# Optimization experiments

Hardware: AMD Instinct MI355X
Metric: run time of the kernel (lower is better)

The kernel has to match this reference:

```python
import jax, jax.numpy as jnp
import numpy as np

B, N, A = 8, 16384, 7
NUM_GROUP = 1024   # npoint / G
GROUP_SIZE = 32    # knn k / M


def setup_inputs() -> dict:
    key = jax.random.key(0)
    xyz = jax.random.uniform(key, (B, N, A), dtype=jnp.float32)
    return {"xyz": xyz}


def _farthest_point_sample(xyz, npoint):
    # xyz: [B, N, A]; distances computed on first 3 dims only.
    b, n, a = xyz.shape
    coords = xyz[:, :, :3]
    batch = jnp.arange(b)
    # Deterministic start index (original uses randint; any start is a valid FPS seed).
    init = (jnp.full((b, n), 1e10, dtype=xyz.dtype), jnp.zeros((b,), dtype=jnp.int32))

    def step(carry, _):
        distance, farthest = carry
        centroid = xyz[batch, farthest]                      # [B, A]
        d = jnp.sum((coords - centroid[:, None, :3]) ** 2, -1)  # [B, N]
        distance = jnp.minimum(distance, d)                  # masked update == min
        new_farthest = jnp.argmax(distance, axis=-1).astype(jnp.int32)
        return (distance, new_farthest), (farthest, centroid)

    _, (idxs, cents) = jax.lax.scan(step, init, None, length=npoint)
    centroids = jnp.swapaxes(idxs, 0, 1)        # [B, npoint]
    centroids_attrs = jnp.swapaxes(cents, 0, 1)  # [B, npoint, A]
    return centroids, centroids_attrs


def _knn(center, xyz, k):
    # Euclidean cdist over ALL A attributes (as in the original torch.cdist call).
    # Squared distance preserves topk ordering.
    c2 = jnp.sum(center ** 2, -1)[:, :, None]    # [B, G, 1]
    x2 = jnp.sum(xyz ** 2, -1)[:, None, :]       # [B, 1, N]
    d2 = c2 + x2 - 2.0 * jnp.einsum('bga,bna->bgn', center, xyz)  # [B, G, N]
    _, idx = jax.lax.top_k(-d2, k)               # smallest-k, ascending distance
    return idx


def reference(xyz):
    center_idx, centroids_attrs = _farthest_point_sample(xyz, NUM_GROUP)
    centroids_coors = centroids_attrs[:, :, :3]
    idx = _knn(centroids_attrs, xyz, GROUP_SIZE)             # [B, G, M]
    b = xyz.shape[0]
    neighborhood = xyz[jnp.arange(b)[:, None, None], idx]    # [B, G, M, A]
    neighborhood = jnp.concatenate(
        [neighborhood[..., :3] - centroids_coors[:, :, None, :],
         neighborhood[..., 3:]], axis=-1)
    return neighborhood, center_idx, centroids_attrs, centroids_coors
```

## Files before the change

kernel.cpp:

```cpp
#include <hip/hip_runtime.h>

#define N_PTS  16384
#define B_SZ   8
#define NGROUP 1024
#define KNN_K  32
#define ATTR   7

#define OFF_NB     0
#define OFF_IDX    (B_SZ * NGROUP * KNN_K * ATTR)
#define OFF_CATTR  (OFF_IDX + B_SZ * NGROUP)
#define OFF_CCOORD (OFF_CATTR + B_SZ * NGROUP * ATTR)

typedef float v2f __attribute__((ext_vector_type(2)));
typedef float f2u __attribute__((ext_vector_type(2), aligned(4)));

template <int CTRL>
__device__ __forceinline__ float fmax_dpp_step(float x) {
    int d = __builtin_amdgcn_update_dpp(__float_as_int(x), __float_as_int(x),
                                        CTRL, 0xf, 0xf, false);
    return fmaxf(x, __int_as_float(d));
}
template <int CTRL>
__device__ __forceinline__ unsigned umin_dpp_step(unsigned x) {
    unsigned d = (unsigned)__builtin_amdgcn_update_dpp((int)x, (int)x,
                                                       CTRL, 0xf, 0xf, false);
    return x < d ? x : d;
}

__device__ __forceinline__ float wave_max_f32(float x) {
    x = fmax_dpp_step<0x111>(x);
    x = fmax_dpp_step<0x112>(x);
    x = fmax_dpp_step<0x114>(x);
    x = fmax_dpp_step<0x118>(x);
    x = fmax_dpp_step<0x142>(x);
    x = fmax_dpp_step<0x143>(x);
    return __int_as_float(__builtin_amdgcn_readlane(__float_as_int(x), 63));
}
__device__ __forceinline__ unsigned wave_min_u32(unsigned x) {
    x = umin_dpp_step<0x111>(x);
    x = umin_dpp_step<0x112>(x);
    x = umin_dpp_step<0x114>(x);
    x = umin_dpp_step<0x118>(x);
    x = umin_dpp_step<0x142>(x);
    x = umin_dpp_step<0x143>(x);
    return (unsigned)__builtin_amdgcn_readlane((int)x, 63);
}

__global__ void prep_kernel(const float* __restrict__ xyz, float* __restrict__ x2,
                            float* __restrict__ xt) {
#pragma clang fp contract(off)
    int i = blockIdx.x * blockDim.x + threadIdx.x;
    if (i >= B_SZ * N_PTS) return;
    const int b = i >> 14;
    const int p = i & (N_PTS - 1);
    const float* q = xyz + (size_t)i * ATTR;
    f2u a01 = *(const f2u*)q;
    f2u a23 = *(const f2u*)(q + 2);
    f2u a45 = *(const f2u*)(q + 4);
    float a6 = q[6];
    float s = a01.x * a01.x;
    s = s + a01.y * a01.y;
    s = s + a23.x * a23.x;
    s = s + a23.y * a23.y;
    s = s + a45.x * a45.x;
    s = s + a45.y * a45.y;
    s = s + a6 * a6;
    x2[i] = s;
    float* T = xt + (size_t)b * ATTR * N_PTS + p;
    T[0 * N_PTS] = a01.x;
    T[1 * N_PTS] = a01.y;
    T[2 * N_PTS] = a23.x;
    T[3 * N_PTS] = a23.y;
    T[4 * N_PTS] = a45.x;
    T[5 * N_PTS] = a45.y;
    T[6 * N_PTS] = a6;
}

#define FOR8(M) M(0) M(1) M(2) M(3) M(4) M(5) M(6) M(7)

#define PT_DECL(J) v2f px##J, py##J, pz##J, pd##J;

#define PT_LOAD(J) { \
    const int q = t + (J << 10); \
    const float* r0 = X + (size_t)(q << 1) * ATTR; \
    f2u u0 = *(const f2u*)r0;          float z0 = r0[2]; \
    f2u u1 = *(const f2u*)(r0 + ATTR); float z1 = r0[2 + ATTR]; \
    px##J = (v2f){u0.x, u1.x}; \
    py##J = (v2f){u0.y, u1.y}; \
    pz##J = (v2f){z0, z1}; \
    pd##J = (v2f){1e10f, 1e10f}; }

#define PT_STEP(J) { \
    v2f dx = px##J - cx2; \
    v2f dy = py##J - cy2; \
    v2f dz = pz##J - cz2; \
    v2f a  = dx * dx; \
    a = a + dy * dy; \
    a = a + dz * dz; \
    v2f nd; \
    nd.x = fminf(pd##J.x, a.x); \
    nd.y = fminf(pd##J.y, a.y); \
    pd##J = nd; \
    if (nd.x > best) { best = nd.x; bidx = (t << 1) + (J << 11); } \
    if (nd.y > best) { best = nd.y; bidx = (t << 1) + (J << 11) + 1; } }

__global__ __launch_bounds__(1024)
__attribute__((amdgpu_waves_per_eu(4, 4)))
void fps_kernel(const float* __restrict__ xyz, float* __restrict__ out) {
#pragma clang fp contract(off)
    const int b = blockIdx.x;
    const int t = threadIdx.x;
    const int lane = t & 63;
    const int w = t >> 6;
    const float* X = xyz + (size_t)b * N_PTS * ATTR;

    FOR8(PT_DECL)
    FOR8(PT_LOAD)

    __shared__ unsigned long long sbuf[2][16];
    __shared__ int sel[NGROUP];
    if (t == 0) sel[0] = 0;
    float cx = X[0], cy = X[1], cz = X[2];
    __syncthreads();

    for (int s = 0; s < NGROUP - 1; ++s) {
        const int par = s & 1;
        asm volatile("" : "+v"(px0), "+v"(px1), "+v"(px2), "+v"(px3),
                          "+v"(px4), "+v"(px5), "+v"(px6), "+v"(px7));
        asm volatile("" : "+v"(py0), "+v"(py1), "+v"(py2), "+v"(py3),
                          "+v"(py4), "+v"(py5), "+v"(py6), "+v"(py7));
        asm volatile("" : "+v"(pz0), "+v"(pz1), "+v"(pz2), "+v"(pz3),
                          "+v"(pz4), "+v"(pz5), "+v"(pz6), "+v"(pz7));
        const v2f cx2 = {cx, cx}, cy2 = {cy, cy}, cz2 = {cz, cz};
        float best = -1.0f;
        int   bidx = 0;
        FOR8(PT_STEP)
        const float wm = wave_max_f32(best);
        const unsigned cand = (best == wm) ? (unsigned)bidx : 0xFFFFFFFFu;
        const unsigned widx = wave_min_u32(cand);
        if (lane == 0) {
            sbuf[par][w] = ((unsigned long long)__float_as_uint(wm) << 32) |
                           (unsigned)(N_PTS - widx);
        }
        __syncthreads();
        unsigned long long bk = sbuf[par][0];
#pragma unroll
        for (int i = 1; i < 16; ++i) {
            const unsigned long long k = sbuf[par][i];
            if (k > bk) bk = k;
        }
        const int win = N_PTS - (int)(unsigned)bk;
        const int sbidx = __builtin_amdgcn_readfirstlane(win);
        if (t == 0) sel[s + 1] = sbidx;
        const float* q = X + (size_t)sbidx * ATTR;
        cx = q[0]; cy = q[1]; cz = q[2];
    }
    __syncthreads();

    {
        const int g = t;
        const int idx = sel[g];
        const float* q = X + (size_t)idx * ATTR;
        float a0 = q[0], a1 = q[1], a2 = q[2], a3 = q[3], a4 = q[4], a5 = q[5], a6 = q[6];
        out[OFF_IDX + b * NGROUP + g] = (float)idx;
        float* ca = out + OFF_CATTR + (size_t)(b * NGROUP + g) * ATTR;
        ca[0] = a0; ca[1] = a1; ca[2] = a2; ca[3] = a3; ca[4] = a4; ca[5] = a5; ca[6] = a6;
        float* cc = out + OFF_CCOORD + (size_t)(b * NGROUP + g) * 3;
        cc[0] = a0; cc[1] = a1; cc[2] = a2;
    }
}

__device__ __forceinline__ void topk_insert(float d2, int p, int lane,
                                            float& ld, int& li, float& kd, int& ki) {
    const bool cand = (d2 < kd) || (d2 == kd && p < ki);
    unsigned long long mask = __ballot(cand);
    while (mask) {
        const int l = __ffsll(mask) - 1;
        mask &= mask - 1;
        const float dc = __shfl(d2, l);
        const int   pc = __shfl(p, l);
        if ((dc < kd) || (dc == kd && pc < ki)) {
            const bool before = (ld < dc) || (ld == dc && li < pc);
            const int pos = (int)__popcll(__ballot(before));
            const float sd = __shfl_up(ld, 1);
            const int   si = __shfl_up(li, 1);
            if (lane == pos)      { ld = dc; li = pc; }
            else if (lane > pos)  { ld = sd; li = si; }
            if (lane >= KNN_K)    { ld = __builtin_inff(); li = 0x7fffffff; }
            kd = __shfl(ld, KNN_K - 1);
            ki = __shfl(li, KNN_K - 1);
        }
    }
}

__global__ __launch_bounds__(256) void knn_kernel(const float* __restrict__ xyz,
                                                  const float* __restrict__ x2,
                                                  const float* __restrict__ xt,
                                                  float* __restrict__ out) {
#pragma clang fp contract(off)
    const int lane = threadIdx.x & 63;
    const int gg = blockIdx.x * 4 + (threadIdx.x >> 6);
    const int b  = gg >> 10;
    const float* X = xyz + (size_t)b * N_PTS * ATTR;

    const float* C = out + OFF_CATTR + (size_t)gg * ATTR;
    const float c0 = C[0], c1 = C[1], c2a = C[2], c3 = C[3], c4 = C[4], c5 = C[5], c6 = C[6];
    float csq = c0 * c0;
    csq = csq + c1 * c1;
    csq = csq + c2a * c2a;
    csq = csq + c3 * c3;
    csq = csq + c4 * c4;
    csq = csq + c5 * c5;
    csq = csq + c6 * c6;

    float ld = __builtin_inff();
    int   li = 0x7fffffff;
    float kd = __builtin_inff();
    int   ki = 0x7fffffff;

    if (xt != nullptr) {
        const float* T0 = xt + (size_t)b * ATTR * N_PTS;
        const float* T1 = T0 + N_PTS;
        const float* T2 = T1 + N_PTS;
        const float* T3 = T2 + N_PTS;
        const float* T4 = T3 + N_PTS;
        const float* T5 = T4 + N_PTS;
        const float* T6 = T5 + N_PTS;
        const float* XB = x2 + (size_t)b * N_PTS;
        for (int p0 = 0; p0 < N_PTS; p0 += 64) {
            const int p = p0 + lane;
            const float q0 = T0[p], q1 = T1[p], q2 = T2[p], q3 = T3[p];
            const float q4 = T4[p], q5 = T5[p], q6 = T6[p];
            float dot = c0 * q0;
            dot = dot + c1 * q1;
            dot = dot + c2a * q2;
            dot = dot + c3 * q3;
            dot = dot + c4 * q4;
            dot = dot + c5 * q5;
            dot = dot + c6 * q6;
            const float xx = XB[p];
            const float d2 = (csq + xx) - 2.0f * dot;
            topk_insert(d2, p, lane, ld, li, kd, ki);
        }
    } else {
        for (int p0 = 0; p0 < N_PTS; p0 += 64) {
            const int p = p0 + lane;
            const float* q = X + (size_t)p * ATTR;
            float dot = c0 * q[0];
            dot = dot + c1 * q[1];
            dot = dot + c2a * q[2];
            dot = dot + c3 * q[3];
            dot = dot + c4 * q[4];
            dot = dot + c5 * q[5];
            dot = dot + c6 * q[6];
            float xx = q[0] * q[0];
            xx = xx + q[1] * q[1];
            xx = xx + q[2] * q[2];
            xx = xx + q[3] * q[3];
            xx = xx + q[4] * q[4];
            xx = xx + q[5] * q[5];
            xx = xx + q[6] * q[6];
            const float d2 = (csq + xx) - 2.0f * dot;
            topk_insert(d2, p, lane, ld, li, kd, ki);
        }
    }

    if (lane < KNN_K) {
        const float* q = X + (size_t)li * ATTR;
        float* o = out + OFF_NB + ((size_t)gg * KNN_K + lane) * ATTR;
        o[0] = q[0] - c0;
        o[1] = q[1] - c1;
        o[2] = q[2] - c2a;
        o[3] = q[3];
        o[4] = q[4];
        o[5] = q[5];
        o[6] = q[6];
    }
}

extern "C" void kernel_launch(void* const* d_in, const int* in_sizes, int n_in,
                              void* d_out, int out_size, void* d_ws, size_t ws_size,
                              hipStream_t stream) {
    const float* xyz = (const float*)d_in[0];
    float* out = (float*)d_out;

    const size_t need = (size_t)(B_SZ * N_PTS) * (1 + ATTR) * sizeof(float);
    const bool use_ws = ws_size >= need;
    float* x2 = use_ws ? (float*)d_ws : nullptr;
    float* xt = use_ws ? ((float*)d_ws + B_SZ * N_PTS) : nullptr;

    if (use_ws) {
        prep_kernel<<<(B_SZ * N_PTS + 255) / 256, 256, 0, stream>>>(xyz, x2, xt);
    }
    fps_kernel<<<B_SZ, 1024, 0, stream>>>(xyz, out);
    knn_kernel<<<(B_SZ * NGROUP) / 4, 256, 0, stream>>>(xyz, x2, xt, out);
}
```

Baseline: 2.056 ms.

## Stage FPS xy coords in LDS and reduce block max via LDS atomicMax

Moves the x/y coordinates of each thread's points out of registers into a shared-memory float4 array, keeping only z and the running distances in registers, and drops the waves-per-eu occupancy attribute. It also replaces the per-wave slot array and 16-entry serial scan with a single 64-bit LDS atomicMax into a triple-buffered slot that thread 0 clears one step ahead. The goal is a shorter critical path per FPS iteration and lower register pressure. In exchange, every step now reads 8 float4 values from LDS per thread, and the 16 atomics to one address serialize.

```diff
diff --git a/kernel.cpp b/kernel.cpp
--- a/kernel.cpp
+++ b/kernel.cpp
@@ -12,6 +12,7 @@
 #define OFF_CCOORD (OFF_CATTR + B_SZ * NGROUP * ATTR)
 
 typedef float v2f __attribute__((ext_vector_type(2)));
+typedef float v4f __attribute__((ext_vector_type(4)));
 typedef float f2u __attribute__((ext_vector_type(2), aligned(4)));
 
 template <int CTRL>
@@ -78,21 +79,21 @@
 
 #define FOR8(M) M(0) M(1) M(2) M(3) M(4) M(5) M(6) M(7)
 
-#define PT_DECL(J) v2f px##J, py##J, pz##J, pd##J;
-
-#define PT_LOAD(J) { \
+#define PT_DECL(J) v2f pz##J, pd##J;
+
+#define STAGE(J) { \
     const int q = t + (J << 10); \
     const float* r0 = X + (size_t)(q << 1) * ATTR; \
     f2u u0 = *(const f2u*)r0;          float z0 = r0[2]; \
     f2u u1 = *(const f2u*)(r0 + ATTR); float z1 = r0[2 + ATTR]; \
-    px##J = (v2f){u0.x, u1.x}; \
-    py##J = (v2f){u0.y, u1.y}; \
+    lxy[q] = (v4f){u0.x, u1.x, u0.y, u1.y}; \
     pz##J = (v2f){z0, z1}; \
     pd##J = (v2f){1e10f, 1e10f}; }
 
 #define PT_STEP(J) { \
-    v2f dx = px##J - cx2; \
-    v2f dy = py##J - cy2; \
+    const v4f xy = lxy[t + (J << 10)]; \
+    v2f dx = (v2f){xy.x, xy.y} - cx2; \
+    v2f dy = (v2f){xy.z, xy.w} - cy2; \
     v2f dz = pz##J - cz2; \
     v2f a  = dx * dx; \
     a = a + dy * dy; \
@@ -105,32 +106,25 @@
     if (nd.y > best) { best = nd.y; bidx = (t << 1) + (J << 11) + 1; } }
 
 __global__ __launch_bounds__(1024)
-__attribute__((amdgpu_waves_per_eu(4, 4)))
 void fps_kernel(const float* __restrict__ xyz, float* __restrict__ out) {
 #pragma clang fp contract(off)
     const int b = blockIdx.x;
     const int t = threadIdx.x;
     const int lane = t & 63;
-    const int w = t >> 6;
     const float* X = xyz + (size_t)b * N_PTS * ATTR;
 
+    __shared__ v4f lxy[N_PTS / 2];
+    __shared__ int sel[NGROUP];
+    __shared__ unsigned long long slot[3];
+
     FOR8(PT_DECL)
-    FOR8(PT_LOAD)
-
-    __shared__ unsigned long long sbuf[2][16];
-    __shared__ int sel[NGROUP];
-    if (t == 0) sel[0] = 0;
+    FOR8(STAGE)
+
+    if (t == 0) { slot[0] = 0ull; sel[0] = 0; }
     float cx = X[0], cy = X[1], cz = X[2];
     __syncthreads();
 
     for (int s = 0; s < NGROUP - 1; ++s) {
-        const int par = s & 1;
-        asm volatile("" : "+v"(px0), "+v"(px1), "+v"(px2), "+v"(px3),
-                          "+v"(px4), "+v"(px5), "+v"(px6), "+v"(px7));
-        asm volatile("" : "+v"(py0), "+v"(py1), "+v"(py2), "+v"(py3),
-                          "+v"(py4), "+v"(py5), "+v"(py6), "+v"(py7));
-        asm volatile("" : "+v"(pz0), "+v"(pz1), "+v"(pz2), "+v"(pz3),
-                          "+v"(pz4), "+v"(pz5), "+v"(pz6), "+v"(pz7));
         const v2f cx2 = {cx, cx}, cy2 = {cy, cy}, cz2 = {cz, cz};
         float best = -1.0f;
         int   bidx = 0;
@@ -139,16 +133,14 @@
         const unsigned cand = (best == wm) ? (unsigned)bidx : 0xFFFFFFFFu;
         const unsigned widx = wave_min_u32(cand);
         if (lane == 0) {
-            sbuf[par][w] = ((unsigned long long)__float_as_uint(wm) << 32) |
-                           (unsigned)(N_PTS - widx);
-        }
+            const unsigned long long key =
+                ((unsigned long long)__float_as_uint(wm) << 32) |
+                (unsigned)(N_PTS - widx);
+            atomicMax(&slot[s % 3], key);
+        }
+        if (t == 0) slot[(s + 1) % 3] = 0ull;
         __syncthreads();
-        unsigned long long bk = sbuf[par][0];
-#pragma unroll
-        for (int i = 1; i < 16; ++i) {
-            const unsigned long long k = sbuf[par][i];
-            if (k > bk) bk = k;
-        }
+        const unsigned long long bk = slot[s % 3];
         const int win = N_PTS - (int)(unsigned)bk;
         const int sbidx = __builtin_amdgcn_readfirstlane(win);
         if (t == 0) sel[s + 1] = sbidx;
```

Result: no change. 2.036 ms (-1.0%).
